# Performance work log

Hardware: AMD Instinct MI355X
Metric: run time of the kernel (lower is better)

The kernel has to match this reference:

```python
import jax, jax.numpy as jnp
import numpy as np

NUM_NODES = 50000
NUM_EDGES = 640000
IN_FEAT = 128
OUT_FEAT = 128


def setup_inputs() -> dict:
    key = jax.random.key(0)
    k1, k2, k3, k4 = jax.random.split(key, 4)
    features = jax.random.normal(k1, (NUM_NODES, IN_FEAT), dtype=jnp.float32)
    weight = jax.random.normal(k2, (IN_FEAT, OUT_FEAT), dtype=jnp.float32) * (1.0 / np.sqrt(IN_FEAT))
    edges_dst = jax.random.randint(k3, (NUM_EDGES,), 0, NUM_NODES, dtype=jnp.int32)
    edges_src = jax.random.randint(k4, (NUM_EDGES,), 0, NUM_NODES, dtype=jnp.int32)
    return {"features": features, "weight": weight, "edges_dst": edges_dst, "edges_src": edges_src}


def reference(features, weight, edges_dst, edges_src):
    # nodes_representation = features @ W   -> [N, out_feat]
    nodes_representation = jnp.matmul(features, weight)

    # gather neighbor (source) features: [E, in_feat]
    neighbour = features[edges_src]

    # unsorted_segment_mean over target node ids (edges_dst)
    seg_sum = jax.ops.segment_sum(neighbour, edges_dst, num_segments=NUM_NODES)
    counts = jax.ops.segment_sum(jnp.ones((NUM_EDGES,), dtype=features.dtype),
                                 edges_dst, num_segments=NUM_NODES)
    aggregated = jnp.where(counts[:, None] > 0, seg_sum / jnp.maximum(counts[:, None], 1.0), 0.0)

    aggregated_messages = jnp.matmul(aggregated, weight)  # [N, out_feat]

    # combination_type == 'concat', activation == 'relu'
    h = jnp.concatenate([nodes_representation, aggregated_messages], axis=-1)  # [N, 2*out_feat]
    return jax.nn.relu(h)
```

## Files before the change

### kernel.cpp

```cpp
#include <hip/hip_runtime.h>

#define FEAT 128
#define NPB 50
#define NB 1000
#define MAGIC50 85899346u
#define CELL 16
#define CAP 48
#define SBLK 512
#define CVB 512
#define SB_STRIDE 136
#define GEMB 782

typedef __attribute__((ext_vector_type(8))) short bhalf8;
typedef __attribute__((ext_vector_type(4))) float floatx4;

__device__ __forceinline__ unsigned int cvtpk(float lo, float hi) {
    unsigned int r;
    asm("v_cvt_pk_bf16_f32 %0, %1, %2" : "=v"(r) : "v"(lo), "v"(hi));
    return r;
}

__global__ __launch_bounds__(256, 2) void scatter_kernel(
    const int* __restrict__ edst, const int* __restrict__ esrc,
    unsigned int* __restrict__ binned, int nE)
{
    __shared__ __align__(16) unsigned int lbin[NB * CELL];
    __shared__ unsigned int cur32[NB / 4];

    const int tid = threadIdx.x;
    const int blk = blockIdx.x;

    for (int i = tid; i < NB / 4; i += 256) cur32[i] = 0u;
    __syncthreads();

    const int nE4 = nE >> 2;
    const int perBlk = (nE4 + SBLK - 1) / SBLK;
    const int gBeg = blk * perBlk;
    const int gEnd = min(gBeg + perBlk, nE4);

    for (int g = gBeg + tid; g < gEnd; g += 256) {
        int4 d = *(const int4*)&edst[g << 2];
        int4 s = *(const int4*)&esrc[g << 2];
        #pragma unroll
        for (int e = 0; e < 4; ++e) {
            int dd = (e == 0) ? d.x : (e == 1) ? d.y : (e == 2) ? d.z : d.w;
            int ss = (e == 0) ? s.x : (e == 1) ? s.y : (e == 2) ? s.z : s.w;
            unsigned int bin = __umulhi((unsigned int)dd, MAGIC50);
            int local = dd - (int)bin * NPB;
            const int sh = (bin & 3) * 8;
            unsigned int old = atomicAdd(&cur32[bin >> 2], 1u << sh);
            int slot = (int)((old >> sh) & 0xffu);
            if (slot < CELL - 1)
                lbin[bin * CELL + 1 + slot] =
                    ((unsigned int)local << 16) | (unsigned int)(ss & 0xffff);
        }
    }
    if (blk == 0) {
        for (int i = (nE4 << 2) + tid; i < nE; i += 256) {
            int dd = edst[i], ss = esrc[i];
            unsigned int bin = __umulhi((unsigned int)dd, MAGIC50);
            int local = dd - (int)bin * NPB;
            const int sh = (bin & 3) * 8;
            unsigned int old = atomicAdd(&cur32[bin >> 2], 1u << sh);
            int slot = (int)((old >> sh) & 0xffu);
            if (slot < CELL - 1)
                lbin[bin * CELL + 1 + slot] =
                    ((unsigned int)local << 16) | (unsigned int)(ss & 0xffff);
        }
    }
    __syncthreads();

    for (int bin = tid; bin < NB; bin += 256) {
        unsigned int c = (cur32[bin >> 2] >> ((bin & 3) * 8)) & 0xffu;
        lbin[bin * CELL] = min(c, (unsigned int)(CELL - 1));
    }
    __syncthreads();

    unsigned int* dst = &binned[(size_t)blk * (NB * CELL)];
    for (int i4 = tid; i4 < (NB * CELL) / 4; i4 += 256)
        *(uint4*)&dst[i4 * 4] = *(const uint4*)&lbin[i4 * 4];
}

__global__ __launch_bounds__(256, 4) void wide_kernel(
    const float* __restrict__ feat, const float* __restrict__ W,
    unsigned short* __restrict__ FB, unsigned short* __restrict__ WB,
    float* __restrict__ out, int nrows)
{
    __shared__ char smem[128 * SB_STRIDE * 2];
    const int tid = threadIdx.x;

    if (blockIdx.x >= GEMB) {
        if (blockIdx.x < GEMB + CVB) {
            const int cb = blockIdx.x - GEMB;
            const size_t total = (size_t)nrows * (FEAT / 8);
            for (size_t g = (size_t)cb * 256 + tid; g < total; g += (size_t)CVB * 256) {
                const float* fp = &feat[g * 8];
                float4 f0 = *(const float4*)fp;
                float4 f1 = *(const float4*)(fp + 4);
                uint4 p;
                p.x = cvtpk(f0.x, f0.y);
                p.y = cvtpk(f0.z, f0.w);
                p.z = cvtpk(f1.x, f1.y);
                p.w = cvtpk(f1.z, f1.w);
                *(uint4*)&FB[g * 8] = p;
            }
            return;
        }
        for (int i = tid; i < 2048; i += 256) {
            int n  = i >> 4;
            int k8 = i & 15;
            float f[8];
            #pragma unroll
            for (int t = 0; t < 8; ++t) f[t] = W[(size_t)(k8 * 8 + t) * FEAT + n];
            uint4 p;
            p.x = cvtpk(f[0], f[1]);
            p.y = cvtpk(f[2], f[3]);
            p.z = cvtpk(f[4], f[5]);
            p.w = cvtpk(f[6], f[7]);
            *(uint4*)&WB[n * FEAT + k8 * 8] = p;
        }
        return;
    }

    unsigned short* sB = (unsigned short*)smem;
    const int bx   = blockIdx.x;
    const int wave = tid >> 6;
    const int lane = tid & 63;
    const int m    = lane & 15;
    const int kg   = lane >> 4;

    for (int i = tid; i < 2048; i += 256) {
        int n  = i & 127;
        int kc = i >> 7;
        const float* wp = &W[(size_t)(kc * 8) * FEAT + n];
        float f[8];
        #pragma unroll
        for (int t = 0; t < 8; ++t) f[t] = wp[(size_t)t * FEAT];
        uint4 p;
        p.x = cvtpk(f[0], f[1]);
        p.y = cvtpk(f[2], f[3]);
        p.z = cvtpk(f[4], f[5]);
        p.w = cvtpk(f[6], f[7]);
        *(uint4*)&sB[n * SB_STRIDE + kc * 8] = p;
    }

    const int row  = bx * 64 + wave * 16 + m;
    const int rowc = min(row, nrows - 1);
    bhalf8 afrag[4];
    {
        const float* ap = &feat[(size_t)rowc * FEAT + kg * 8];
        #pragma unroll
        for (int ks = 0; ks < 4; ++ks) {
            float4 f0 = *(const float4*)&ap[ks * 32];
            float4 f1 = *(const float4*)&ap[ks * 32 + 4];
            union { bhalf8 v; unsigned int u[4]; } a;
            a.u[0] = cvtpk(f0.x, f0.y);
            a.u[1] = cvtpk(f0.z, f0.w);
            a.u[2] = cvtpk(f1.x, f1.y);
            a.u[3] = cvtpk(f1.z, f1.w);
            afrag[ks] = a.v;
        }
    }
    __syncthreads();

    floatx4 acc[8];
    #pragma unroll
    for (int nt = 0; nt < 8; ++nt) acc[nt] = (floatx4){0.f, 0.f, 0.f, 0.f};

    #pragma unroll
    for (int ks = 0; ks < 4; ++ks) {
        #pragma unroll
        for (int nt = 0; nt < 8; ++nt) {
            bhalf8 bb = *(bhalf8*)&sB[(nt * 16 + m) * SB_STRIDE + ks * 32 + kg * 8];
            acc[nt] = __builtin_amdgcn_mfma_f32_16x16x32_bf16(afrag[ks], bb, acc[nt], 0, 0, 0);
        }
    }

    const int rbase = bx * 64 + wave * 16 + kg * 4;
    #pragma unroll
    for (int i = 0; i < 4; ++i) {
        int r = rbase + i;
        if (r < nrows) {
            #pragma unroll
            for (int nt = 0; nt < 8; ++nt)
                out[(size_t)r * (2 * FEAT) + nt * 16 + m] = fmaxf(acc[nt][i], 0.f);
        }
    }
}

__global__ __launch_bounds__(256, 6) void gather_kernel(
    const unsigned short* __restrict__ FB, const unsigned short* __restrict__ WB,
    const unsigned int* __restrict__ binned, float* __restrict__ out, int nrows)
{
    __shared__ int lcnt[NPB];
    __shared__ unsigned short lbkt[NPB * CAP];
    __shared__ unsigned short smean[64 * SB_STRIDE];

    const int bin = blockIdx.x;
    const int tid = threadIdx.x;

    for (int i = tid; i < NPB; i += 256) lcnt[i] = 0;
    __syncthreads();

    for (int c = tid; c < SBLK; c += 256) {
        const size_t base = (size_t)c * (NB * CELL) + (size_t)bin * CELL;
        const int cnt = (int)binned[base];
        for (int k = 0; k < cnt; ++k) {
            unsigned int u = binned[base + 1 + k];
            int local = (int)(u >> 16);
            int slot = atomicAdd(&lcnt[local], 1);
            if (slot < CAP) lbkt[local * CAP + slot] = (unsigned short)(u & 0xffffu);
        }
    }
    __syncthreads();

    const int lane = tid & 63;
    const int wave = tid >> 6;
    const int g  = lane >> 4;
    const int cl = lane & 15;
    const int m  = lane & 15;
    const int kg = lane >> 4;

    for (int lA = wave; lA < NPB; lA += 8) {
        const int lB = lA + 4;
        const bool okB = lB < NPB;
        const int degA = min(lcnt[lA], CAP);
        const int degB = okB ? min(lcnt[lB], CAP) : 0;

        float a[8], b[8];
        #pragma unroll
        for (int t = 0; t < 8; ++t) { a[t] = 0.f; b[t] = 0.f; }

        int idxA = (lane < degA) ? (int)lbkt[lA * CAP + lane] : 0;
        int idxB = (lane < degB) ? (int)lbkt[lB * CAP + lane] : 0;

        const int itMax = (max(degA, degB) + 3) >> 2;
        for (int it = 0; it < itMax; ++it) {
            const int jg = it * 4 + g;
            const int sA = __shfl(idxA, jg);
            const int sX = __shfl(idxB, jg);
            uint4 vA = make_uint4(0u, 0u, 0u, 0u);
            uint4 vB = make_uint4(0u, 0u, 0u, 0u);
            if (jg < degA) vA = *(const uint4*)&FB[(size_t)sA * FEAT + cl * 8];
            if (jg < degB) vB = *(const uint4*)&FB[(size_t)sX * FEAT + cl * 8];
            a[0] += __uint_as_float(vA.x << 16);
            a[1] += __uint_as_float(vA.x & 0xffff0000u);
            a[2] += __uint_as_float(vA.y << 16);
            a[3] += __uint_as_float(vA.y & 0xffff0000u);
            a[4] += __uint_as_float(vA.z << 16);
            a[5] += __uint_as_float(vA.z & 0xffff0000u);
            a[6] += __uint_as_float(vA.w << 16);
            a[7] += __uint_as_float(vA.w & 0xffff0000u);
            b[0] += __uint_as_float(vB.x << 16);
            b[1] += __uint_as_float(vB.x & 0xffff0000u);
            b[2] += __uint_as_float(vB.y << 16);
            b[3] += __uint_as_float(vB.y & 0xffff0000u);
            b[4] += __uint_as_float(vB.z << 16);
            b[5] += __uint_as_float(vB.z & 0xffff0000u);
            b[6] += __uint_as_float(vB.w << 16);
            b[7] += __uint_as_float(vB.w & 0xffff0000u);
        }

        #pragma unroll
        for (int t = 0; t < 8; ++t) {
            a[t] += __shfl_xor(a[t], 16);
            a[t] += __shfl_xor(a[t], 32);
            b[t] += __shfl_xor(b[t], 16);
            b[t] += __shfl_xor(b[t], 32);
        }

        if (g == 0) {
            const float invA = (degA > 0) ? (1.0f / (float)degA) : 0.0f;
            uint4 p;
            p.x = cvtpk(a[0] * invA, a[1] * invA);
            p.y = cvtpk(a[2] * invA, a[3] * invA);
            p.z = cvtpk(a[4] * invA, a[5] * invA);
            p.w = cvtpk(a[6] * invA, a[7] * invA);
            *(uint4*)&smean[lA * SB_STRIDE + cl * 8] = p;
            if (okB) {
                const float invB = (degB > 0) ? (1.0f / (float)degB) : 0.0f;
                uint4 q;
                q.x = cvtpk(b[0] * invB, b[1] * invB);
                q.y = cvtpk(b[2] * invB, b[3] * invB);
                q.z = cvtpk(b[4] * invB, b[5] * invB);
                q.w = cvtpk(b[6] * invB, b[7] * invB);
                *(uint4*)&smean[lB * SB_STRIDE + cl * 8] = q;
            }
        }
    }
    __syncthreads();

    bhalf8 am[4];
    const int arow = wave * 16 + m;
    #pragma unroll
    for (int ks = 0; ks < 4; ++ks)
        am[ks] = *(bhalf8*)&smean[arow * SB_STRIDE + ks * 32 + kg * 8];

    floatx4 acc[8];
    #pragma unroll
    for (int nt = 0; nt < 8; ++nt) acc[nt] = (floatx4){0.f, 0.f, 0.f, 0.f};

    #pragma unroll
    for (int ks = 0; ks < 4; ++ks) {
        #pragma unroll
        for (int nt = 0; nt < 8; ++nt) {
            bhalf8 bb = *(const bhalf8*)&WB[(size_t)(nt * 16 + m) * FEAT + ks * 32 + kg * 8];
            acc[nt] = __builtin_amdgcn_mfma_f32_16x16x32_bf16(am[ks], bb, acc[nt], 0, 0, 0);
        }
    }

    const int lbase = wave * 16 + kg * 4;
    #pragma unroll
    for (int i = 0; i < 4; ++i) {
        int local = lbase + i;
        int node = bin * NPB + local;
        if (local < NPB && node < nrows) {
            #pragma unroll
            for (int nt = 0; nt < 8; ++nt)
                out[(size_t)node * (2 * FEAT) + FEAT + nt * 16 + m] =
                    fmaxf(acc[nt][i], 0.f);
        }
    }
}

extern "C" void kernel_launch(void* const* d_in, const int* in_sizes, int n_in,
                              void* d_out, int out_size, void* d_ws, size_t ws_size,
                              hipStream_t stream)
{
    const float* feat = (const float*)d_in[0];
    const float* W    = (const float*)d_in[1];
    const int* edst   = (const int*)d_in[2];
    const int* esrc   = (const int*)d_in[3];
    float* out        = (float*)d_out;

    const int N = in_sizes[0] / FEAT;
    const int E = in_sizes[2];

    char* ws = (char*)d_ws;
    unsigned short* FB = (unsigned short*)ws;
    size_t off = (size_t)N * FEAT * sizeof(unsigned short);
    off = (off + 63) & ~(size_t)63;
    unsigned int* binned = (unsigned int*)(ws + off);
    off += (size_t)SBLK * NB * CELL * 4;
    off = (off + 63) & ~(size_t)63;
    unsigned short* WB = (unsigned short*)(ws + off);
    off += (size_t)FEAT * FEAT * sizeof(unsigned short);

    scatter_kernel<<<SBLK, 256, 0, stream>>>(edst, esrc, binned, E);

    wide_kernel<<<GEMB + CVB + 1, 256, 0, stream>>>(feat, W, FB, WB, out, N);

    gather_kernel<<<NB, 256, 0, stream>>>(FB, WB, binned, out, N);
}
```

Baseline: 155.6 us.

## Merge three launches into prep and fused gather/GEMM kernels with transposed bin layout

Scatter binning, the bf16 conversion of features and the conversion of W now run as role-split blocks in one prep kernel. A second kernel interleaves the dense GEMM blocks, which now read pre-converted bf16 features and W, with the gather/mean/GEMM blocks. Scatter block count is halved, and the binned layout is transposed so each gather block reads one contiguous strip. The intent is to cut a launch boundary, fill the device with mixed work, and coalesce the gather's bin reads. The trade-off is that halving the scatter blocks doubles the edges per block, which raises per-cell overflow pressure (cells cap at 15 edges) and could drop edges.

```diff
diff --git a/kernel.cpp b/kernel.cpp
--- a/kernel.cpp
+++ b/kernel.cpp
@@ -6,7 +6,7 @@
 #define MAGIC50 85899346u
 #define CELL 16
 #define CAP 48
-#define SBLK 512
+#define SBLK 256
 #define CVB 512
 #define SB_STRIDE 136
 #define GEMB 782
@@ -20,146 +20,271 @@
     return r;
 }
 
-__global__ __launch_bounds__(256, 2) void scatter_kernel(
+__global__ __launch_bounds__(256, 2) void prep_kernel(
+    const float* __restrict__ feat, const float* __restrict__ W,
     const int* __restrict__ edst, const int* __restrict__ esrc,
-    unsigned int* __restrict__ binned, int nE)
+    unsigned short* __restrict__ FB, unsigned short* __restrict__ WB,
+    unsigned int* __restrict__ binned, int nrows, int nE)
 {
     __shared__ __align__(16) unsigned int lbin[NB * CELL];
     __shared__ unsigned int cur32[NB / 4];
 
     const int tid = threadIdx.x;
-    const int blk = blockIdx.x;
-
-    for (int i = tid; i < NB / 4; i += 256) cur32[i] = 0u;
-    __syncthreads();
-
-    const int nE4 = nE >> 2;
-    const int perBlk = (nE4 + SBLK - 1) / SBLK;
-    const int gBeg = blk * perBlk;
-    const int gEnd = min(gBeg + perBlk, nE4);
-
-    for (int g = gBeg + tid; g < gEnd; g += 256) {
-        int4 d = *(const int4*)&edst[g << 2];
-        int4 s = *(const int4*)&esrc[g << 2];
-        #pragma unroll
-        for (int e = 0; e < 4; ++e) {
-            int dd = (e == 0) ? d.x : (e == 1) ? d.y : (e == 2) ? d.z : d.w;
-            int ss = (e == 0) ? s.x : (e == 1) ? s.y : (e == 2) ? s.z : s.w;
-            unsigned int bin = __umulhi((unsigned int)dd, MAGIC50);
-            int local = dd - (int)bin * NPB;
-            const int sh = (bin & 3) * 8;
-            unsigned int old = atomicAdd(&cur32[bin >> 2], 1u << sh);
-            int slot = (int)((old >> sh) & 0xffu);
-            if (slot < CELL - 1)
-                lbin[bin * CELL + 1 + slot] =
-                    ((unsigned int)local << 16) | (unsigned int)(ss & 0xffff);
-        }
-    }
-    if (blk == 0) {
-        for (int i = (nE4 << 2) + tid; i < nE; i += 256) {
-            int dd = edst[i], ss = esrc[i];
-            unsigned int bin = __umulhi((unsigned int)dd, MAGIC50);
-            int local = dd - (int)bin * NPB;
-            const int sh = (bin & 3) * 8;
-            unsigned int old = atomicAdd(&cur32[bin >> 2], 1u << sh);
-            int slot = (int)((old >> sh) & 0xffu);
-            if (slot < CELL - 1)
-                lbin[bin * CELL + 1 + slot] =
-                    ((unsigned int)local << 16) | (unsigned int)(ss & 0xffff);
-        }
-    }
-    __syncthreads();
-
-    for (int bin = tid; bin < NB; bin += 256) {
-        unsigned int c = (cur32[bin >> 2] >> ((bin & 3) * 8)) & 0xffu;
-        lbin[bin * CELL] = min(c, (unsigned int)(CELL - 1));
-    }
-    __syncthreads();
-
-    unsigned int* dst = &binned[(size_t)blk * (NB * CELL)];
-    for (int i4 = tid; i4 < (NB * CELL) / 4; i4 += 256)
-        *(uint4*)&dst[i4 * 4] = *(const uint4*)&lbin[i4 * 4];
-}
-
-__global__ __launch_bounds__(256, 4) void wide_kernel(
-    const float* __restrict__ feat, const float* __restrict__ W,
-    unsigned short* __restrict__ FB, unsigned short* __restrict__ WB,
-    float* __restrict__ out, int nrows)
-{
-    __shared__ char smem[128 * SB_STRIDE * 2];
-    const int tid = threadIdx.x;
-
-    if (blockIdx.x >= GEMB) {
-        if (blockIdx.x < GEMB + CVB) {
-            const int cb = blockIdx.x - GEMB;
-            const size_t total = (size_t)nrows * (FEAT / 8);
-            for (size_t g = (size_t)cb * 256 + tid; g < total; g += (size_t)CVB * 256) {
-                const float* fp = &feat[g * 8];
-                float4 f0 = *(const float4*)fp;
-                float4 f1 = *(const float4*)(fp + 4);
-                uint4 p;
-                p.x = cvtpk(f0.x, f0.y);
-                p.y = cvtpk(f0.z, f0.w);
-                p.z = cvtpk(f1.x, f1.y);
-                p.w = cvtpk(f1.z, f1.w);
-                *(uint4*)&FB[g * 8] = p;
-            }
-            return;
-        }
-        for (int i = tid; i < 2048; i += 256) {
-            int n  = i >> 4;
-            int k8 = i & 15;
-            float f[8];
-            #pragma unroll
-            for (int t = 0; t < 8; ++t) f[t] = W[(size_t)(k8 * 8 + t) * FEAT + n];
+
+    if (blockIdx.x < SBLK) {
+        const int blk = blockIdx.x;
+        for (int i = tid; i < NB / 4; i += 256) cur32[i] = 0u;
+        __syncthreads();
+
+        const int nE4 = nE >> 2;
+        const int perBlk = (nE4 + SBLK - 1) / SBLK;
+        const int gBeg = blk * perBlk;
+        const int gEnd = min(gBeg + perBlk, nE4);
+
+        for (int g = gBeg + tid; g < gEnd; g += 256) {
+            int4 d = *(const int4*)&edst[g << 2];
+            int4 s = *(const int4*)&esrc[g << 2];
+            #pragma unroll
+            for (int e = 0; e < 4; ++e) {
+                int dd = (e == 0) ? d.x : (e == 1) ? d.y : (e == 2) ? d.z : d.w;
+                int ss = (e == 0) ? s.x : (e == 1) ? s.y : (e == 2) ? s.z : s.w;
+                unsigned int bin = __umulhi((unsigned int)dd, MAGIC50);
+                int local = dd - (int)bin * NPB;
+                const int sh = (bin & 3) * 8;
+                unsigned int old = atomicAdd(&cur32[bin >> 2], 1u << sh);
+                int slot = (int)((old >> sh) & 0xffu);
+                if (slot < CELL - 1)
+                    lbin[bin * CELL + 1 + slot] =
+                        ((unsigned int)local << 16) | (unsigned int)(ss & 0xffff);
+            }
+        }
+        if (blk == 0) {
+            for (int i = (nE4 << 2) + tid; i < nE; i += 256) {
+                int dd = edst[i], ss = esrc[i];
+                unsigned int bin = __umulhi((unsigned int)dd, MAGIC50);
+                int local = dd - (int)bin * NPB;
+                const int sh = (bin & 3) * 8;
+                unsigned int old = atomicAdd(&cur32[bin >> 2], 1u << sh);
+                int slot = (int)((old >> sh) & 0xffu);
+                if (slot < CELL - 1)
+                    lbin[bin * CELL + 1 + slot] =
+                        ((unsigned int)local << 16) | (unsigned int)(ss & 0xffff);
+            }
+        }
+        __syncthreads();
+
+        for (int bin = tid; bin < NB; bin += 256) {
+            unsigned int c = (cur32[bin >> 2] >> ((bin & 3) * 8)) & 0xffu;
+            lbin[bin * CELL] = min(c, (unsigned int)(CELL - 1));
+        }
+        __syncthreads();
+
+        const int lane = tid & 63;
+        const int wv   = tid >> 6;
+        const int q    = lane & 3;
+        for (int cg = wv * 16 + (lane >> 2); cg < NB; cg += 64) {
+            uint4 v = *(const uint4*)&lbin[cg * CELL + q * 4];
+            *(uint4*)&binned[((size_t)cg * SBLK + blk) * CELL + q * 4] = v;
+        }
+        return;
+    }
+
+    if (blockIdx.x < SBLK + CVB) {
+        const int cb = blockIdx.x - SBLK;
+        const size_t total = (size_t)nrows * (FEAT / 8);
+        for (size_t g = (size_t)cb * 256 + tid; g < total; g += (size_t)CVB * 256) {
+            const float* fp = &feat[g * 8];
+            float4 f0 = *(const float4*)fp;
+            float4 f1 = *(const float4*)(fp + 4);
             uint4 p;
-            p.x = cvtpk(f[0], f[1]);
-            p.y = cvtpk(f[2], f[3]);
-            p.z = cvtpk(f[4], f[5]);
-            p.w = cvtpk(f[6], f[7]);
-            *(uint4*)&WB[n * FEAT + k8 * 8] = p;
+            p.x = cvtpk(f0.x, f0.y);
+            p.y = cvtpk(f0.z, f0.w);
+            p.z = cvtpk(f1.x, f1.y);
+            p.w = cvtpk(f1.z, f1.w);
+            *(uint4*)&FB[g * 8] = p;
         }
         return;
     }
 
-    unsigned short* sB = (unsigned short*)smem;
-    const int bx   = blockIdx.x;
-    const int wave = tid >> 6;
-    const int lane = tid & 63;
-    const int m    = lane & 15;
-    const int kg   = lane >> 4;
-
     for (int i = tid; i < 2048; i += 256) {
-        int n  = i & 127;
-        int kc = i >> 7;
-        const float* wp = &W[(size_t)(kc * 8) * FEAT + n];
+        int n  = i >> 4;
+        int k8 = i & 15;
         float f[8];
         #pragma unroll
-        for (int t = 0; t < 8; ++t) f[t] = wp[(size_t)t * FEAT];
+        for (int t = 0; t < 8; ++t) f[t] = W[(size_t)(k8 * 8 + t) * FEAT + n];
         uint4 p;
         p.x = cvtpk(f[0], f[1]);
         p.y = cvtpk(f[2], f[3]);
         p.z = cvtpk(f[4], f[5]);
         p.w = cvtpk(f[6], f[7]);
-        *(uint4*)&sB[n * SB_STRIDE + kc * 8] = p;
+        *(uint4*)&WB[n * FEAT + k8 * 8] = p;
+    }
+}
+
+__global__ __launch_bounds__(256, 4) void main_kernel(
+    const unsigned short* __restrict__ FB, const unsigned short* __restrict__ WB,
+    const unsigned int* __restrict__ binned, float* __restrict__ out, int nrows)
+{
+    __shared__ char smem[34816];
+
+    const int tid  = threadIdx.x;
+    const int bid  = blockIdx.x;
+    const int wave = tid >> 6;
+    const int lane = tid & 63;
+    const int m    = lane & 15;
+    const int kg   = lane >> 4;
+
+    bool isGather;
+    int rid;
+    if (bid < 2 * GEMB) { isGather = (bid & 1); rid = bid >> 1; }
+    else                { isGather = true;      rid = GEMB + (bid - 2 * GEMB); }
+
+    if (isGather) {
+        const int bin = rid;
+        int* lcnt = (int*)smem;
+        unsigned short* lbkt  = (unsigned short*)(smem + 256);
+        unsigned short* smean = (unsigned short*)(smem + 5120);
+
+        for (int i = tid; i < NPB; i += 256) lcnt[i] = 0;
+        __syncthreads();
+
+        {
+            const unsigned int* strip = &binned[(size_t)bin * SBLK * CELL];
+            const unsigned int* cell = &strip[tid * CELL];
+            const int cnt = (int)cell[0];
+            for (int k = 0; k < cnt; ++k) {
+                unsigned int u = cell[1 + k];
+                int local = (int)(u >> 16);
+                int slot = atomicAdd(&lcnt[local], 1);
+                if (slot < CAP) lbkt[local * CAP + slot] = (unsigned short)(u & 0xffffu);
+            }
+        }
+        __syncthreads();
+
+        const int g  = lane >> 4;
+        const int cl = lane & 15;
+
+        for (int lA = wave; lA < NPB; lA += 8) {
+            const int lB = lA + 4;
+            const bool okB = lB < NPB;
+            const int degA = min(lcnt[lA], CAP);
+            const int degB = okB ? min(lcnt[lB], CAP) : 0;
+
+            float a[8], b[8];
+            #pragma unroll
+            for (int t = 0; t < 8; ++t) { a[t] = 0.f; b[t] = 0.f; }
+
+            int idxA = (lane < degA) ? (int)lbkt[lA * CAP + lane] : 0;
+            int idxB = (lane < degB) ? (int)lbkt[lB * CAP + lane] : 0;
+
+            const int itMax = (max(degA, degB) + 3) >> 2;
+            for (int it = 0; it < itMax; ++it) {
+                const int jg = it * 4 + g;
+                const int sA = __shfl(idxA, jg);
+                const int sX = __shfl(idxB, jg);
+                uint4 vA = make_uint4(0u, 0u, 0u, 0u);
+                uint4 vB = make_uint4(0u, 0u, 0u, 0u);
+                if (jg < degA) vA = *(const uint4*)&FB[(size_t)sA * FEAT + cl * 8];
+                if (jg < degB) vB = *(const uint4*)&FB[(size_t)sX * FEAT + cl * 8];
+                a[0] += __uint_as_float(vA.x << 16);
+                a[1] += __uint_as_float(vA.x & 0xffff0000u);
+                a[2] += __uint_as_float(vA.y << 16);
+                a[3] += __uint_as_float(vA.y & 0xffff0000u);
+                a[4] += __uint_as_float(vA.z << 16);
+                a[5] += __uint_as_float(vA.z & 0xffff0000u);
+                a[6] += __uint_as_float(vA.w << 16);
+                a[7] += __uint_as_float(vA.w & 0xffff0000u);
+                b[0] += __uint_as_float(vB.x << 16);
+                b[1] += __uint_as_float(vB.x & 0xffff0000u);
+                b[2] += __uint_as_float(vB.y << 16);
+                b[3] += __uint_as_float(vB.y & 0xffff0000u);
+                b[4] += __uint_as_float(vB.z << 16);
+                b[5] += __uint_as_float(vB.z & 0xffff0000u);
+                b[6] += __uint_as_float(vB.w << 16);
+                b[7] += __uint_as_float(vB.w & 0xffff0000u);
+            }
+
+            #pragma unroll
+            for (int t = 0; t < 8; ++t) {
+                a[t] += __shfl_xor(a[t], 16);
+                a[t] += __shfl_xor(a[t], 32);
+                b[t] += __shfl_xor(b[t], 16);
+                b[t] += __shfl_xor(b[t], 32);
+            }
+
+            if (g == 0) {
+                const float invA = (degA > 0) ? (1.0f / (float)degA) : 0.0f;
+                uint4 p;
+                p.x = cvtpk(a[0] * invA, a[1] * invA);
+                p.y = cvtpk(a[2] * invA, a[3] * invA);
+                p.z = cvtpk(a[4] * invA, a[5] * invA);
+                p.w = cvtpk(a[6] * invA, a[7] * invA);
+                *(uint4*)&smean[lA * SB_STRIDE + cl * 8] = p;
+                if (okB) {
+                    const float invB = (degB > 0) ? (1.0f / (float)degB) : 0.0f;
+                    uint4 q;
+                    q.x = cvtpk(b[0] * invB, b[1] * invB);
+                    q.y = cvtpk(b[2] * invB, b[3] * invB);
+                    q.z = cvtpk(b[4] * invB, b[5] * invB);
+                    q.w = cvtpk(b[6] * invB, b[7] * invB);
+                    *(uint4*)&smean[lB * SB_STRIDE + cl * 8] = q;
+                }
+            }
+        }
+        __syncthreads();
+
+        bhalf8 am[4];
+        const int arow = wave * 16 + m;
+        #pragma unroll
+        for (int ks = 0; ks < 4; ++ks)
+            am[ks] = *(bhalf8*)&smean[arow * SB_STRIDE + ks * 32 + kg * 8];
+
+        floatx4 acc[8];
+        #pragma unroll
+        for (int nt = 0; nt < 8; ++nt) acc[nt] = (floatx4){0.f, 0.f, 0.f, 0.f};
+
+        #pragma unroll
+        for (int ks = 0; ks < 4; ++ks) {
+            #pragma unroll
+            for (int nt = 0; nt < 8; ++nt) {
+                bhalf8 bb = *(const bhalf8*)&WB[(size_t)(nt * 16 + m) * FEAT + ks * 32 + kg * 8];
+                acc[nt] = __builtin_amdgcn_mfma_f32_16x16x32_bf16(am[ks], bb, acc[nt], 0, 0, 0);
+            }
+        }
+
+        const int lbase = wave * 16 + kg * 4;
+        #pragma unroll
+        for (int i = 0; i < 4; ++i) {
+            int local = lbase + i;
+            int node = bin * NPB + local;
+            if (local < NPB && node < nrows) {
+                #pragma unroll
+                for (int nt = 0; nt < 8; ++nt)
+                    out[(size_t)node * (2 * FEAT) + FEAT + nt * 16 + m] =
+                        fmaxf(acc[nt][i], 0.f);
+            }
+        }
+        return;
+    }
+
+    unsigned short* sB = (unsigned short*)smem;
+    const int bx = rid;
+
+    for (int i = tid; i < 2048; i += 256) {
+        uint4 p = *(const uint4*)&WB[i * 8];
+        int n  = i >> 4;
+        int k8 = i & 15;
+        *(uint4*)&sB[n * SB_STRIDE + k8 * 8] = p;
     }
 
     const int row  = bx * 64 + wave * 16 + m;
     const int rowc = min(row, nrows - 1);
     bhalf8 afrag[4];
     {
-        const float* ap = &feat[(size_t)rowc * FEAT + kg * 8];
-        #pragma unroll
-        for (int ks = 0; ks < 4; ++ks) {
-            float4 f0 = *(const float4*)&ap[ks * 32];
-            float4 f1 = *(const float4*)&ap[ks * 32 + 4];
-            union { bhalf8 v; unsigned int u[4]; } a;
-            a.u[0] = cvtpk(f0.x, f0.y);
-            a.u[1] = cvtpk(f0.z, f0.w);
-            a.u[2] = cvtpk(f1.x, f1.y);
-            a.u[3] = cvtpk(f1.z, f1.w);
-            afrag[ks] = a.v;
-        }
+        const unsigned short* ap = &FB[(size_t)rowc * FEAT + kg * 8];
+        #pragma unroll
+        for (int ks = 0; ks < 4; ++ks)
+            afrag[ks] = *(const bhalf8*)&ap[ks * 32];
     }
     __syncthreads();
 
@@ -184,141 +309,6 @@
             #pragma unroll
             for (int nt = 0; nt < 8; ++nt)
                 out[(size_t)r * (2 * FEAT) + nt * 16 + m] = fmaxf(acc[nt][i], 0.f);
-        }
-    }
-}
-
-__global__ __launch_bounds__(256, 6) void gather_kernel(
-    const unsigned short* __restrict__ FB, const unsigned short* __restrict__ WB,
-    const unsigned int* __restrict__ binned, float* __restrict__ out, int nrows)
-{
-    __shared__ int lcnt[NPB];
-    __shared__ unsigned short lbkt[NPB * CAP];
-    __shared__ unsigned short smean[64 * SB_STRIDE];
-
-    const int bin = blockIdx.x;
-    const int tid = threadIdx.x;
-
-    for (int i = tid; i < NPB; i += 256) lcnt[i] = 0;
-    __syncthreads();
-
-    for (int c = tid; c < SBLK; c += 256) {
-        const size_t base = (size_t)c * (NB * CELL) + (size_t)bin * CELL;
-        const int cnt = (int)binned[base];
-        for (int k = 0; k < cnt; ++k) {
-            unsigned int u = binned[base + 1 + k];
-            int local = (int)(u >> 16);
-            int slot = atomicAdd(&lcnt[local], 1);
-            if (slot < CAP) lbkt[local * CAP + slot] = (unsigned short)(u & 0xffffu);
-        }
-    }
-    __syncthreads();
-
-    const int lane = tid & 63;
-    const int wave = tid >> 6;
-    const int g  = lane >> 4;
-    const int cl = lane & 15;
-    const int m  = lane & 15;
-    const int kg = lane >> 4;
-
-    for (int lA = wave; lA < NPB; lA += 8) {
-        const int lB = lA + 4;
-        const bool okB = lB < NPB;
-        const int degA = min(lcnt[lA], CAP);
-        const int degB = okB ? min(lcnt[lB], CAP) : 0;
-
-        float a[8], b[8];
-        #pragma unroll
-        for (int t = 0; t < 8; ++t) { a[t] = 0.f; b[t] = 0.f; }
-
-        int idxA = (lane < degA) ? (int)lbkt[lA * CAP + lane] : 0;
-        int idxB = (lane < degB) ? (int)lbkt[lB * CAP + lane] : 0;
-
-        const int itMax = (max(degA, degB) + 3) >> 2;
-        for (int it = 0; it < itMax; ++it) {
-            const int jg = it * 4 + g;
-            const int sA = __shfl(idxA, jg);
-            const int sX = __shfl(idxB, jg);
-            uint4 vA = make_uint4(0u, 0u, 0u, 0u);
-            uint4 vB = make_uint4(0u, 0u, 0u, 0u);
-            if (jg < degA) vA = *(const uint4*)&FB[(size_t)sA * FEAT + cl * 8];
-            if (jg < degB) vB = *(const uint4*)&FB[(size_t)sX * FEAT + cl * 8];
-            a[0] += __uint_as_float(vA.x << 16);
-            a[1] += __uint_as_float(vA.x & 0xffff0000u);
-            a[2] += __uint_as_float(vA.y << 16);
-            a[3] += __uint_as_float(vA.y & 0xffff0000u);
-            a[4] += __uint_as_float(vA.z << 16);
-            a[5] += __uint_as_float(vA.z & 0xffff0000u);
-            a[6] += __uint_as_float(vA.w << 16);
-            a[7] += __uint_as_float(vA.w & 0xffff0000u);
-            b[0] += __uint_as_float(vB.x << 16);
-            b[1] += __uint_as_float(vB.x & 0xffff0000u);
-            b[2] += __uint_as_float(vB.y << 16);
-            b[3] += __uint_as_float(vB.y & 0xffff0000u);
-            b[4] += __uint_as_float(vB.z << 16);
-            b[5] += __uint_as_float(vB.z & 0xffff0000u);
-            b[6] += __uint_as_float(vB.w << 16);
-            b[7] += __uint_as_float(vB.w & 0xffff0000u);
-        }
-
-        #pragma unroll
-        for (int t = 0; t < 8; ++t) {
-            a[t] += __shfl_xor(a[t], 16);
-            a[t] += __shfl_xor(a[t], 32);
-            b[t] += __shfl_xor(b[t], 16);
-            b[t] += __shfl_xor(b[t], 32);
-        }
-
-        if (g == 0) {
-            const float invA = (degA > 0) ? (1.0f / (float)degA) : 0.0f;
-            uint4 p;
-            p.x = cvtpk(a[0] * invA, a[1] * invA);
-            p.y = cvtpk(a[2] * invA, a[3] * invA);
-            p.z = cvtpk(a[4] * invA, a[5] * invA);
-            p.w = cvtpk(a[6] * invA, a[7] * invA);
-            *(uint4*)&smean[lA * SB_STRIDE + cl * 8] = p;
-            if (okB) {
-                const float invB = (degB > 0) ? (1.0f / (float)degB) : 0.0f;
-                uint4 q;
-                q.x = cvtpk(b[0] * invB, b[1] * invB);
-                q.y = cvtpk(b[2] * invB, b[3] * invB);
-                q.z = cvtpk(b[4] * invB, b[5] * invB);
-                q.w = cvtpk(b[6] * invB, b[7] * invB);
-                *(uint4*)&smean[lB * SB_STRIDE + cl * 8] = q;
-            }
-        }
-    }
-    __syncthreads();
-
-    bhalf8 am[4];
-    const int arow = wave * 16 + m;
-    #pragma unroll
-    for (int ks = 0; ks < 4; ++ks)
-        am[ks] = *(bhalf8*)&smean[arow * SB_STRIDE + ks * 32 + kg * 8];
-
-    floatx4 acc[8];
-    #pragma unroll
-    for (int nt = 0; nt < 8; ++nt) acc[nt] = (floatx4){0.f, 0.f, 0.f, 0.f};
-
-    #pragma unroll
-    for (int ks = 0; ks < 4; ++ks) {
-        #pragma unroll
-        for (int nt = 0; nt < 8; ++nt) {
-            bhalf8 bb = *(const bhalf8*)&WB[(size_t)(nt * 16 + m) * FEAT + ks * 32 + kg * 8];
-            acc[nt] = __builtin_amdgcn_mfma_f32_16x16x32_bf16(am[ks], bb, acc[nt], 0, 0, 0);
-        }
-    }
-
-    const int lbase = wave * 16 + kg * 4;
-    #pragma unroll
-    for (int i = 0; i < 4; ++i) {
-        int local = lbase + i;
-        int node = bin * NPB + local;
-        if (local < NPB && node < nrows) {
-            #pragma unroll
-            for (int nt = 0; nt < 8; ++nt)
-                out[(size_t)node * (2 * FEAT) + FEAT + nt * 16 + m] =
-                    fmaxf(acc[nt][i], 0.f);
         }
     }
 }
@@ -341,14 +331,13 @@
     size_t off = (size_t)N * FEAT * sizeof(unsigned short);
     off = (off + 63) & ~(size_t)63;
     unsigned int* binned = (unsigned int*)(ws + off);
-    off += (size_t)SBLK * NB * CELL * 4;
+    off += (size_t)NB * SBLK * CELL * 4;
     off = (off + 63) & ~(size_t)63;
     unsigned short* WB = (unsigned short*)(ws + off);
     off += (size_t)FEAT * FEAT * sizeof(unsigned short);
 
-    scatter_kernel<<<SBLK, 256, 0, stream>>>(edst, esrc, binned, E);
-
-    wide_kernel<<<GEMB + CVB + 1, 256, 0, stream>>>(feat, W, FB, WB, out, N);
-
-    gather_kernel<<<NB, 256, 0, stream>>>(FB, WB, binned, out, N);
+    prep_kernel<<<SBLK + CVB + 1, 256, 0, stream>>>(
+        feat, W, edst, esrc, FB, WB, binned, N, E);
+
+    main_kernel<<<NB + GEMB, 256, 0, stream>>>(FB, WB, binned, out, N);
 }
```

Result: slower. 171.0 us (+9.9%).

## Transpose binned edge layout to bin-major and regroup gather into 16-lane node groups

Applied to the files above, without the earlier changes.

The scatter kernel now writes its per-bin cells in bin-major order, so each gather block reads one contiguous slab of cells instead of strided cells spread across the whole buffer. The number of scatter blocks is halved, so one gather thread handles exactly one cell. The mean-aggregation loop now gives each node to a 16-thread group that issues four independent row loads per iteration, with no shuffle-based index broadcast or cross-lane reductions. The trade-offs are more edges per scatter block, which raises the risk of the 15-slot cells overflowing, and less load parallelism per node when degrees are low.

```diff
diff --git a/kernel.cpp b/kernel.cpp
--- a/kernel.cpp
+++ b/kernel.cpp
@@ -6,7 +6,7 @@
 #define MAGIC50 85899346u
 #define CELL 16
 #define CAP 48
-#define SBLK 512
+#define SBLK 256
 #define CVB 512
 #define SB_STRIDE 136
 #define GEMB 782
@@ -18,6 +18,17 @@
     unsigned int r;
     asm("v_cvt_pk_bf16_f32 %0, %1, %2" : "=v"(r) : "v"(lo), "v"(hi));
     return r;
+}
+
+__device__ __forceinline__ void acc8(float* a, uint4 v) {
+    a[0] += __uint_as_float(v.x << 16);
+    a[1] += __uint_as_float(v.x & 0xffff0000u);
+    a[2] += __uint_as_float(v.y << 16);
+    a[3] += __uint_as_float(v.y & 0xffff0000u);
+    a[4] += __uint_as_float(v.z << 16);
+    a[5] += __uint_as_float(v.z & 0xffff0000u);
+    a[6] += __uint_as_float(v.w << 16);
+    a[7] += __uint_as_float(v.w & 0xffff0000u);
 }
 
 __global__ __launch_bounds__(256, 2) void scatter_kernel(
@@ -76,9 +87,13 @@
     }
     __syncthreads();
 
-    unsigned int* dst = &binned[(size_t)blk * (NB * CELL)];
-    for (int i4 = tid; i4 < (NB * CELL) / 4; i4 += 256)
-        *(uint4*)&dst[i4 * 4] = *(const uint4*)&lbin[i4 * 4];
+    const int lane = tid & 63;
+    const int wv   = tid >> 6;
+    const int q    = lane & 3;
+    for (int cg = wv * 16 + (lane >> 2); cg < NB; cg += 64) {
+        uint4 v = *(const uint4*)&lbin[cg * CELL + q * 4];
+        *(uint4*)&binned[((size_t)cg * SBLK + blk) * CELL + q * 4] = v;
+    }
 }
 
 __global__ __launch_bounds__(256, 4) void wide_kernel(
@@ -202,11 +217,11 @@
     for (int i = tid; i < NPB; i += 256) lcnt[i] = 0;
     __syncthreads();
 
-    for (int c = tid; c < SBLK; c += 256) {
-        const size_t base = (size_t)c * (NB * CELL) + (size_t)bin * CELL;
-        const int cnt = (int)binned[base];
+    {
+        const unsigned int* cell = &binned[((size_t)bin * SBLK + tid) * CELL];
+        const int cnt = (int)cell[0];
         for (int k = 0; k < cnt; ++k) {
-            unsigned int u = binned[base + 1 + k];
+            unsigned int u = cell[1 + k];
             int local = (int)(u >> 16);
             int slot = atomicAdd(&lcnt[local], 1);
             if (slot < CAP) lbkt[local * CAP + slot] = (unsigned short)(u & 0xffffu);
@@ -214,81 +229,48 @@
     }
     __syncthreads();
 
+    const int qw = tid >> 4;
+    const int cl = tid & 15;
+
+    for (int l = qw; l < NPB; l += 16) {
+        const int deg = min(lcnt[l], CAP);
+        float acc[8];
+        #pragma unroll
+        for (int t = 0; t < 8; ++t) acc[t] = 0.f;
+
+        const unsigned short* bkt = &lbkt[l * CAP];
+        for (int j0 = 0; j0 < deg; j0 += 4) {
+            int s0 = (int)bkt[j0];
+            int s1 = (j0 + 1 < deg) ? (int)bkt[j0 + 1] : s0;
+            int s2 = (j0 + 2 < deg) ? (int)bkt[j0 + 2] : s0;
+            int s3 = (j0 + 3 < deg) ? (int)bkt[j0 + 3] : s0;
+            uint4 v0 = *(const uint4*)&FB[(size_t)s0 * FEAT + cl * 8];
+            uint4 v1 = *(const uint4*)&FB[(size_t)s1 * FEAT + cl * 8];
+            uint4 v2 = *(const uint4*)&FB[(size_t)s2 * FEAT + cl * 8];
+            uint4 v3 = *(const uint4*)&FB[(size_t)s3 * FEAT + cl * 8];
+            if (j0 + 1 >= deg) v1 = make_uint4(0u, 0u, 0u, 0u);
+            if (j0 + 2 >= deg) v2 = make_uint4(0u, 0u, 0u, 0u);
+            if (j0 + 3 >= deg) v3 = make_uint4(0u, 0u, 0u, 0u);
+            acc8(acc, v0);
+            acc8(acc, v1);
+            acc8(acc, v2);
+            acc8(acc, v3);
+        }
+
+        const float inv = (deg > 0) ? (1.0f / (float)deg) : 0.0f;
+        uint4 p;
+        p.x = cvtpk(acc[0] * inv, acc[1] * inv);
+        p.y = cvtpk(acc[2] * inv, acc[3] * inv);
+        p.z = cvtpk(acc[4] * inv, acc[5] * inv);
+        p.w = cvtpk(acc[6] * inv, acc[7] * inv);
+        *(uint4*)&smean[l * SB_STRIDE + cl * 8] = p;
+    }
+    __syncthreads();
+
+    const int wave = tid >> 6;
     const int lane = tid & 63;
-    const int wave = tid >> 6;
-    const int g  = lane >> 4;
-    const int cl = lane & 15;
-    const int m  = lane & 15;
-    const int kg = lane >> 4;
-
-    for (int lA = wave; lA < NPB; lA += 8) {
-        const int lB = lA + 4;
-        const bool okB = lB < NPB;
-        const int degA = min(lcnt[lA], CAP);
-        const int degB = okB ? min(lcnt[lB], CAP) : 0;
-
-        float a[8], b[8];
-        #pragma unroll
-        for (int t = 0; t < 8; ++t) { a[t] = 0.f; b[t] = 0.f; }
-
-        int idxA = (lane < degA) ? (int)lbkt[lA * CAP + lane] : 0;
-        int idxB = (lane < degB) ? (int)lbkt[lB * CAP + lane] : 0;
-
-        const int itMax = (max(degA, degB) + 3) >> 2;
-        for (int it = 0; it < itMax; ++it) {
-            const int jg = it * 4 + g;
-            const int sA = __shfl(idxA, jg);
-            const int sX = __shfl(idxB, jg);
-            uint4 vA = make_uint4(0u, 0u, 0u, 0u);
-            uint4 vB = make_uint4(0u, 0u, 0u, 0u);
-            if (jg < degA) vA = *(const uint4*)&FB[(size_t)sA * FEAT + cl * 8];
-            if (jg < degB) vB = *(const uint4*)&FB[(size_t)sX * FEAT + cl * 8];
-            a[0] += __uint_as_float(vA.x << 16);
-            a[1] += __uint_as_float(vA.x & 0xffff0000u);
-            a[2] += __uint_as_float(vA.y << 16);
-            a[3] += __uint_as_float(vA.y & 0xffff0000u);
-            a[4] += __uint_as_float(vA.z << 16);
-            a[5] += __uint_as_float(vA.z & 0xffff0000u);
-            a[6] += __uint_as_float(vA.w << 16);
-            a[7] += __uint_as_float(vA.w & 0xffff0000u);
-            b[0] += __uint_as_float(vB.x << 16);
-            b[1] += __uint_as_float(vB.x & 0xffff0000u);
-            b[2] += __uint_as_float(vB.y << 16);
-            b[3] += __uint_as_float(vB.y & 0xffff0000u);
-            b[4] += __uint_as_float(vB.z << 16);
-            b[5] += __uint_as_float(vB.z & 0xffff0000u);
-            b[6] += __uint_as_float(vB.w << 16);
-            b[7] += __uint_as_float(vB.w & 0xffff0000u);
-        }
-
-        #pragma unroll
-        for (int t = 0; t < 8; ++t) {
-            a[t] += __shfl_xor(a[t], 16);
-            a[t] += __shfl_xor(a[t], 32);
-            b[t] += __shfl_xor(b[t], 16);
-            b[t] += __shfl_xor(b[t], 32);
-        }
-
-        if (g == 0) {
-            const float invA = (degA > 0) ? (1.0f / (float)degA) : 0.0f;
-            uint4 p;
-            p.x = cvtpk(a[0] * invA, a[1] * invA);
-            p.y = cvtpk(a[2] * invA, a[3] * invA);
-            p.z = cvtpk(a[4] * invA, a[5] * invA);
-            p.w = cvtpk(a[6] * invA, a[7] * invA);
-            *(uint4*)&smean[lA * SB_STRIDE + cl * 8] = p;
-            if (okB) {
-                const float invB = (degB > 0) ? (1.0f / (float)degB) : 0.0f;
-                uint4 q;
-                q.x = cvtpk(b[0] * invB, b[1] * invB);
-                q.y = cvtpk(b[2] * invB, b[3] * invB);
-                q.z = cvtpk(b[4] * invB, b[5] * invB);
-                q.w = cvtpk(b[6] * invB, b[7] * invB);
-                *(uint4*)&smean[lB * SB_STRIDE + cl * 8] = q;
-            }
-        }
-    }
-    __syncthreads();
+    const int m    = lane & 15;
+    const int kg   = lane >> 4;
 
     bhalf8 am[4];
     const int arow = wave * 16 + m;
@@ -341,7 +323,7 @@
     size_t off = (size_t)N * FEAT * sizeof(unsigned short);
     off = (off + 63) & ~(size_t)63;
     unsigned int* binned = (unsigned int*)(ws + off);
-    off += (size_t)SBLK * NB * CELL * 4;
+    off += (size_t)NB * SBLK * CELL * 4;
     off = (off + 63) & ~(size_t)63;
     unsigned short* WB = (unsigned short*)(ws + off);
     off += (size_t)FEAT * FEAT * sizeof(unsigned short);
```

New measurement: 144.3 us. 1.08x faster.
